# Performance work log

Hardware: AMD Instinct MI355X
Metric: run time of the kernel (lower is better)

## Reference

```python
import jax, jax.numpy as jnp
import numpy as np

D_K = 64  # d_model=512 // n_heads=8, hardcoded in source
NEG = -1e9


def setup_inputs() -> dict:
    key = jax.random.key(0)
    kq, kk, kv, km = jax.random.split(key, 4)
    B, H, S, D = 2, 8, 2048, D_K
    Q = jax.random.normal(kq, (B, H, S, D), dtype=jnp.float32)
    K = jax.random.normal(kk, (B, H, S, D), dtype=jnp.float32)
    V = jax.random.normal(kv, (B, H, S, D), dtype=jnp.float32)
    attn_mask = jax.random.randint(km, (B, H, S, S), 0, 2).astype(jnp.bool_)
    return {"Q": Q, "K": K, "V": V, "attn_mask": attn_mask}


def reference(Q, K, V, attn_mask):
    # scores = Q @ (K^T / sqrt(d_k))  -- scale applied to K^T as in source
    scale = 1.0 / np.sqrt(D_K).astype(np.float32)
    scores = jnp.einsum('bhqd,bhkd->bhqk', Q, K * scale)
    scores = jnp.where(attn_mask, NEG, scores)
    attn = jax.nn.softmax(scores, axis=-1)
    context = jnp.einsum('bhqk,bhkd->bhqd', attn, V)
    return (context, attn)
```

## Files before the change

kernel.cpp:

```cpp
#include <hip/hip_runtime.h>

typedef float f32x4 __attribute__((ext_vector_type(4)));
typedef _Float16 f16x4 __attribute__((ext_vector_type(4)));
typedef unsigned int u32x4 __attribute__((ext_vector_type(4)));
typedef __bf16 bf16x8_t __attribute__((ext_vector_type(8)));
typedef __bf16 bf16x4_t __attribute__((ext_vector_type(4)));

#define DEVFN static __device__ __forceinline__

constexpr int BHN = 16;
constexpr int SN  = 2048;
constexpr int DN  = 64;
constexpr size_t CTXN = (size_t)BHN * SN * DN;
constexpr int NK1 = 4;
constexpr int NK2 = 4;

DEVFN void qk4_mfma(f32x4& dA, f32x4& dB, bf16x8_t k0v, bf16x8_t k1v,
                    bf16x8_t qA0, bf16x8_t qA1, bf16x8_t qB0, bf16x8_t qB1) {
  asm volatile("s_nop 3\n\t"
               "v_mfma_f32_16x16x32_bf16 %0, %2, %4, %0\n\t"
               "v_mfma_f32_16x16x32_bf16 %1, %2, %6, %1\n\t"
               "v_mfma_f32_16x16x32_bf16 %0, %3, %5, %0\n\t"
               "v_mfma_f32_16x16x32_bf16 %1, %3, %7, %1\n\t"
               "s_nop 7\n\ts_nop 7"
               : "+v"(dA), "+v"(dB)
               : "v"(k0v), "v"(k1v), "v"(qA0), "v"(qA1), "v"(qB0), "v"(qB1));
}

DEVFN void pv8_mfma(f32x4& a0, f32x4& a1, f32x4& a2, f32x4& a3,
                    f32x4& b0, f32x4& b1, f32x4& b2, f32x4& b3,
                    bf16x4_t paA, bf16x4_t paB,
                    bf16x4_t v0, bf16x4_t v1, bf16x4_t v2, bf16x4_t v3) {
  asm volatile("s_nop 3\n\t"
               "v_mfma_f32_16x16x16_bf16 %0, %8, %10, %0\n\t"
               "v_mfma_f32_16x16x16_bf16 %4, %9, %10, %4\n\t"
               "v_mfma_f32_16x16x16_bf16 %1, %8, %11, %1\n\t"
               "v_mfma_f32_16x16x16_bf16 %5, %9, %11, %5\n\t"
               "v_mfma_f32_16x16x16_bf16 %2, %8, %12, %2\n\t"
               "v_mfma_f32_16x16x16_bf16 %6, %9, %12, %6\n\t"
               "v_mfma_f32_16x16x16_bf16 %3, %8, %13, %3\n\t"
               "v_mfma_f32_16x16x16_bf16 %7, %9, %13, %7\n\t"
               "s_nop 7\n\ts_nop 7"
               : "+v"(a0), "+v"(a1), "+v"(a2), "+v"(a3),
                 "+v"(b0), "+v"(b1), "+v"(b2), "+v"(b3)
               : "v"(paA), "v"(paB), "v"(v0), "v"(v1), "v"(v2), "v"(v3));
}

constexpr int PB = 2048, QB = 1024, KB = 1024, VB = 256;

__global__ __launch_bounds__(256) void prep_kernel(
    const void* __restrict__ mraw, unsigned int* __restrict__ bmT,
    const float* __restrict__ Q, const float* __restrict__ K,
    const float* __restrict__ V, __bf16* __restrict__ Qb,
    __bf16* __restrict__ Kb, __bf16* __restrict__ Vt) {
  const int bid = blockIdx.x;
  const int tidl = threadIdx.x;
  if (bid < PB) {
    __shared__ unsigned int sfl;
    if (tidl == 0) sfl = 0;
    __syncthreads();
    {
      unsigned int f = 0;
      const unsigned int* m32 = (const unsigned int*)mraw;
      for (int i = tidl; i < 4096; i += 256) {
        unsigned int w = m32[i];
        if (w == 0x3F800000u) f |= 2u;
        else if (w > 1u) f |= 1u;
      }
      if (f) atomicOr(&sfl, f);
    }
    __syncthreads();
    const unsigned int fl = (sfl & 2u) ? 2u : ((sfl & 1u) ? 1u : 0u);
    const int tid = bid * 256 + tidl;
    const int NT  = PB * 256;
    if (fl != 1u) {
      const int W = BHN * (SN / 32) * SN;
      const unsigned int* m32 = (const unsigned int*)mraw;
      for (int w = tid; w < W; w += NT) {
        const int q   = w & (SN - 1);
        const int kc2 = (w >> 11) & (SN / 32 - 1);
        const int bh  = w >> 17;
        const unsigned int* src = m32 + ((size_t)(bh * SN + q) * SN) + kc2 * 32;
        unsigned int r = 0;
        #pragma unroll
        for (int j = 0; j < 8; ++j) {
          u32x4 v = *(const u32x4*)(src + j * 4);
          r |= ((unsigned)(v[0] != 0u)) << (4 * j)
             | ((unsigned)(v[1] != 0u)) << (4 * j + 1)
             | ((unsigned)(v[2] != 0u)) << (4 * j + 2)
             | ((unsigned)(v[3] != 0u)) << (4 * j + 3);
        }
        bmT[w] = r;
      }
    } else {
      const int W4 = BHN * (SN / 128) * SN;
      const unsigned char* m8 = (const unsigned char*)mraw;
      for (int w4 = tid; w4 < W4; w4 += NT) {
        const int q   = w4 & (SN - 1);
        const int kc8 = (w4 >> 11) & (SN / 128 - 1);
        const int bh  = w4 >> 15;
        const unsigned char* src = m8 + ((size_t)(bh * SN + q) * SN) + kc8 * 128;
        #pragma unroll
        for (int i = 0; i < 4; ++i) {
          const unsigned int* s32 = (const unsigned int*)(src + 32 * i);
          unsigned int r = 0;
          #pragma unroll
          for (int j = 0; j < 8; ++j) {
            unsigned int x = s32[j];
            r |= ((unsigned)((x & 0x000000FFu) != 0u)) << (4 * j)
               | ((unsigned)((x & 0x0000FF00u) != 0u)) << (4 * j + 1)
               | ((unsigned)((x & 0x00FF0000u) != 0u)) << (4 * j + 2)
               | ((unsigned)((x & 0xFF000000u) != 0u)) << (4 * j + 3);
          }
          bmT[((size_t)(bh * (SN / 32) + kc8 * 4 + i)) * SN + q] = r;
        }
      }
    }
  } else if (bid < PB + QB + KB) {
    const bool isK = (bid >= PB + QB);
    const int rb = bid - (isK ? PB + QB : PB);
    const float* src = isK ? K : Q;
    __bf16* dst = isK ? Kb : Qb;
    const float scale = isK ? 0.125f : 1.0f;
    const size_t i = ((size_t)rb * 256 + tidl) * 8;
    f32x4 v0 = *(const f32x4*)(src + i);
    f32x4 v1 = *(const f32x4*)(src + i + 4);
    bf16x8_t o;
    o[0]=(__bf16)(v0[0]*scale); o[1]=(__bf16)(v0[1]*scale);
    o[2]=(__bf16)(v0[2]*scale); o[3]=(__bf16)(v0[3]*scale);
    o[4]=(__bf16)(v1[0]*scale); o[5]=(__bf16)(v1[1]*scale);
    o[6]=(__bf16)(v1[2]*scale); o[7]=(__bf16)(v1[3]*scale);
    *(bf16x8_t*)(dst + i) = o;
  } else {
    const int vb = bid - (PB + QB + KB);
    const int lane = tidl & 63, wv = tidl >> 6;
    const int k0 = ((vb & 15) * 4 + wv) * 32;
    const int bh = vb >> 4;
    const float* src = V + (size_t)bh * SN * DN;
    __bf16* dst = Vt + (((size_t)bh * (SN / 32) + (k0 >> 5)) * DN + lane) * 32;
    bf16x8_t w0, w1, w2, w3;
    #pragma unroll
    for (int i = 0; i < 8; ++i) {
      w0[i] = (__bf16)src[(size_t)(k0 + i) * DN + lane];
      w1[i] = (__bf16)src[(size_t)(k0 + 8 + i) * DN + lane];
      w2[i] = (__bf16)src[(size_t)(k0 + 16 + i) * DN + lane];
      w3[i] = (__bf16)src[(size_t)(k0 + 24 + i) * DN + lane];
    }
    *(bf16x8_t*)(dst)      = w0;
    *(bf16x8_t*)(dst + 8)  = w1;
    *(bf16x8_t*)(dst + 16) = w2;
    *(bf16x8_t*)(dst + 24) = w3;
  }
}

DEVFN void swz_decode(int bid, int& bh, int& c, int& x) {
  const int xcd = bid & 7, s8 = bid >> 3;
  bh = xcd + 8 * (s8 >> 6);
  const int r6 = s8 & 63;
  c = r6 >> 4;
  x = r6 & 15;
}

__global__ __launch_bounds__(256, 4) void attn_l_kernel(
    const __bf16* __restrict__ Qb, const __bf16* __restrict__ Kb,
    const unsigned int* __restrict__ bmT, float* __restrict__ lpart) {
  __shared__ __align__(16) char Ks[2][8192];
  const int tid = threadIdx.x;
  const int lane = tid & 63, wv = tid >> 6;
  const int qr = lane & 15, g = lane >> 4;
  int bh, c, x;
  swz_decode(blockIdx.x, bh, c, x);
  const int q0 = x * 128 + wv * 32;
  const int CS = SN / NK1, kbase = c * CS;
  const int NT = CS / 64;

  const __bf16* Qbb = Qb + (size_t)bh * SN * DN;
  const int qA = q0 + qr, qB = q0 + 16 + qr;
  bf16x8_t qfA0 = *(const bf16x8_t*)(Qbb + (size_t)qA * DN + 8 * g);
  bf16x8_t qfA1 = *(const bf16x8_t*)(Qbb + (size_t)qA * DN + 32 + 8 * g);
  bf16x8_t qfB0 = *(const bf16x8_t*)(Qbb + (size_t)qB * DN + 8 * g);
  bf16x8_t qfB1 = *(const bf16x8_t*)(Qbb + (size_t)qB * DN + 32 + 8 * g);
  const size_t rowA = (size_t)bh * SN + qA;
  const size_t rowB = (size_t)bh * SN + qB;
  const unsigned int* bmb = bmT + (size_t)bh * (SN / 32) * SN;
  const int kb2 = kbase >> 5;

  const int krow = tid >> 2;
  const int kcol = (tid & 3) * 32;
  const int swz  = (krow & 7) << 4;
  const int kdst0 = krow * 128 + ((kcol     ) ^ swz);
  const int kdst1 = krow * 128 + ((kcol + 16) ^ swz);
  const char* Ksrc = (const char*)(Kb + (size_t)bh * SN * DN + (size_t)kbase * DN);

  {
    u32x4 a = *(const u32x4*)(Ksrc + krow * 128 + kcol);
    u32x4 b = *(const u32x4*)(Ksrc + krow * 128 + kcol + 16);
    *(u32x4*)&Ks[0][kdst0] = a;
    *(u32x4*)&Ks[0][kdst1] = b;
  }
  __syncthreads();

  float lA = 0.f, lB = 0.f;
  for (int tt = 0; tt < NT; ++tt) {
    const bool pf = (tt + 1 < NT);
    u32x4 a, b;
    if (pf) {
      a = *(const u32x4*)(Ksrc + (tt + 1) * 8192 + krow * 128 + kcol);
      b = *(const u32x4*)(Ksrc + (tt + 1) * 8192 + krow * 128 + kcol + 16);
    }
    const char* Kbuf = Ks[tt & 1];
    const unsigned int wA0 = bmb[(size_t)(kb2 + 2 * tt    ) * SN + qA];
    const unsigned int wA1 = bmb[(size_t)(kb2 + 2 * tt + 1) * SN + qA];
    const unsigned int wB0 = bmb[(size_t)(kb2 + 2 * tt    ) * SN + qB];
    const unsigned int wB1 = bmb[(size_t)(kb2 + 2 * tt + 1) * SN + qB];
    #pragma unroll
    for (int s = 0; s < 4; ++s) {
      const int rk = 16 * s + qr;
      const int rsw = (rk & 7) << 4;
      bf16x8_t kf0 = *(const bf16x8_t*)&Kbuf[rk * 128 + ((16 * g     ) ^ rsw)];
      bf16x8_t kf1 = *(const bf16x8_t*)&Kbuf[rk * 128 + ((64 + 16 * g) ^ rsw)];
      f32x4 aA = {0,0,0,0}, aB = {0,0,0,0};
      qk4_mfma(aA, aB, kf0, kf1, qfA0, qfA1, qfB0, qfB1);
      const unsigned int wmA = (s < 2) ? wA0 : wA1;
      const unsigned int wmB = (s < 2) ? wB0 : wB1;
      const int sh = (s & 1) * 16 + 4 * g;
      lA += ((wmA >> (sh + 0)) & 1u) ? 0.f : __expf(aA[0]);
      lA += ((wmA >> (sh + 1)) & 1u) ? 0.f : __expf(aA[1]);
      lA += ((wmA >> (sh + 2)) & 1u) ? 0.f : __expf(aA[2]);
      lA += ((wmA >> (sh + 3)) & 1u) ? 0.f : __expf(aA[3]);
      lB += ((wmB >> (sh + 0)) & 1u) ? 0.f : __expf(aB[0]);
      lB += ((wmB >> (sh + 1)) & 1u) ? 0.f : __expf(aB[1]);
      lB += ((wmB >> (sh + 2)) & 1u) ? 0.f : __expf(aB[2]);
      lB += ((wmB >> (sh + 3)) & 1u) ? 0.f : __expf(aB[3]);
    }
    if (pf) {
      char* Kn = Ks[(tt + 1) & 1];
      *(u32x4*)&Kn[kdst0] = a;
      *(u32x4*)&Kn[kdst1] = b;
    }
    __syncthreads();
  }
  lA = lA + __shfl_xor(lA, 16); lA = lA + __shfl_xor(lA, 32);
  lB = lB + __shfl_xor(lB, 16); lB = lB + __shfl_xor(lB, 32);
  if (g == 0) {
    lpart[rowA * NK1 + c] = lA;
    lpart[rowB * NK1 + c] = lB;
  }
}

__global__ __launch_bounds__(256, 4) void attn_out_kernel(
    const __bf16* __restrict__ Qb, const __bf16* __restrict__ Kb,
    const __bf16* __restrict__ Vt, const unsigned int* __restrict__ bmT,
    const float* __restrict__ lpart, _Float16* __restrict__ cp,
    float* __restrict__ attn) {
  __shared__ __align__(16) char Ks[2][4096];
  __shared__ __align__(16) char Vs[2][4096];
  const int tid = threadIdx.x;
  const int lane = tid & 63, wv = tid >> 6;
  const int qr = lane & 15, g = lane >> 4;
  int bh, c, x;
  swz_decode(blockIdx.x, bh, c, x);
  const int q0 = x * 128 + wv * 32;
  const int CS = SN / NK2, kbase = c * CS;
  const int NT = CS / 32;

  const __bf16* Qbb = Qb + (size_t)bh * SN * DN;
  const int qA = q0 + qr, qB = q0 + 16 + qr;
  bf16x8_t qfA0 = *(const bf16x8_t*)(Qbb + (size_t)qA * DN + 8 * g);
  bf16x8_t qfA1 = *(const bf16x8_t*)(Qbb + (size_t)qA * DN + 32 + 8 * g);
  bf16x8_t qfB0 = *(const bf16x8_t*)(Qbb + (size_t)qB * DN + 8 * g);
  bf16x8_t qfB1 = *(const bf16x8_t*)(Qbb + (size_t)qB * DN + 32 + 8 * g);
  const size_t rowA = (size_t)bh * SN + qA;
  const size_t rowB = (size_t)bh * SN + qB;
  f32x4 l4A = *(const f32x4*)(lpart + rowA * NK1);
  f32x4 l4B = *(const f32x4*)(lpart + rowB * NK1);
  const float rlA = 1.0f / (l4A[0] + l4A[1] + l4A[2] + l4A[3]);
  const float rlB = 1.0f / (l4B[0] + l4B[1] + l4B[2] + l4B[3]);
  const unsigned int* bmb = bmT + (size_t)bh * (SN / 32) * SN;
  float* arowA = attn + rowA * SN;
  float* arowB = attn + rowB * SN;

  const int krow = tid >> 3;
  const int kcolb = (tid & 7) * 16;
  const int kdst = krow * 128 + (kcolb ^ ((krow & 7) << 4));
  const char* Ksrc = (const char*)(Kb + (size_t)bh * SN * DN + (size_t)kbase * DN);
  const int vd = tid >> 2;
  const int vkb = (tid & 3) * 16;
  const int vdst0 = vd * 64 + ((vkb    ) ^ ((vd & 7) << 3));
  const int vdst1 = vd * 64 + ((vkb + 8) ^ ((vd & 7) << 3));
  const char* Vsrc = (const char*)Vt + ((size_t)bh * (SN / 32) + (kbase >> 5)) * 4096;

  f32x4 cA0 = {0,0,0,0}, cA1 = {0,0,0,0}, cA2 = {0,0,0,0}, cA3 = {0,0,0,0};
  f32x4 cB0 = {0,0,0,0}, cB1 = {0,0,0,0}, cB2 = {0,0,0,0}, cB3 = {0,0,0,0};

  {
    u32x4 kr = *(const u32x4*)(Ksrc + krow * 128 + kcolb);
    u32x4 vr = *(const u32x4*)(Vsrc + tid * 16);
    *(u32x4*)&Ks[0][kdst] = kr;
    *(unsigned long long*)&Vs[0][vdst0] =
        ((unsigned long long)vr[1] << 32) | vr[0];
    *(unsigned long long*)&Vs[0][vdst1] =
        ((unsigned long long)vr[3] << 32) | vr[2];
  }
  __syncthreads();

  for (int tt = 0; tt < NT; ++tt) {
    const bool pf = (tt + 1 < NT);
    u32x4 kr, vr;
    if (pf) {
      kr = *(const u32x4*)(Ksrc + (tt + 1) * 4096 + krow * 128 + kcolb);
      vr = *(const u32x4*)(Vsrc + (tt + 1) * 4096 + tid * 16);
    }
    const char* Kbuf = Ks[tt & 1];
    const char* Vbuf = Vs[tt & 1];
    const int ktg = kbase + tt * 32;
    const unsigned int wmA = bmb[(size_t)((kbase >> 5) + tt) * SN + qA];
    const unsigned int wmB = bmb[(size_t)((kbase >> 5) + tt) * SN + qB];
    #pragma unroll
    for (int s = 0; s < 2; ++s) {
      const int rk = 16 * s + qr;
      bf16x8_t kf0 = *(const bf16x8_t*)&Kbuf[rk * 128 + ((16 * g     ) ^ ((rk & 7) << 4))];
      bf16x8_t kf1 = *(const bf16x8_t*)&Kbuf[rk * 128 + ((64 + 16 * g) ^ ((rk & 7) << 4))];
      const int vxor = (32 * s + 8 * g) ^ ((qr & 7) << 3);
      bf16x4_t vf0 = *(const bf16x4_t*)&Vbuf[(qr     ) * 64 + vxor];
      bf16x4_t vf1 = *(const bf16x4_t*)&Vbuf[(qr + 16) * 64 + vxor];
      bf16x4_t vf2 = *(const bf16x4_t*)&Vbuf[(qr + 32) * 64 + vxor];
      bf16x4_t vf3 = *(const bf16x4_t*)&Vbuf[(qr + 48) * 64 + vxor];
      f32x4 aA = {0,0,0,0}, aB = {0,0,0,0};
      qk4_mfma(aA, aB, kf0, kf1, qfA0, qfA1, qfB0, qfB1);
      const int sh = 16 * s + 4 * g;
      float pA0 = (((wmA >> (sh + 0)) & 1u) ? 0.f : __expf(aA[0])) * rlA;
      float pA1 = (((wmA >> (sh + 1)) & 1u) ? 0.f : __expf(aA[1])) * rlA;
      float pA2 = (((wmA >> (sh + 2)) & 1u) ? 0.f : __expf(aA[2])) * rlA;
      float pA3 = (((wmA >> (sh + 3)) & 1u) ? 0.f : __expf(aA[3])) * rlA;
      float pB0 = (((wmB >> (sh + 0)) & 1u) ? 0.f : __expf(aB[0])) * rlB;
      float pB1 = (((wmB >> (sh + 1)) & 1u) ? 0.f : __expf(aB[1])) * rlB;
      float pB2 = (((wmB >> (sh + 2)) & 1u) ? 0.f : __expf(aB[2])) * rlB;
      float pB3 = (((wmB >> (sh + 3)) & 1u) ? 0.f : __expf(aB[3])) * rlB;
      *(f32x4*)(arowA + ktg + sh) = (f32x4){pA0, pA1, pA2, pA3};
      *(f32x4*)(arowB + ktg + sh) = (f32x4){pB0, pB1, pB2, pB3};
      bf16x4_t paA = {(__bf16)pA0, (__bf16)pA1, (__bf16)pA2, (__bf16)pA3};
      bf16x4_t paB = {(__bf16)pB0, (__bf16)pB1, (__bf16)pB2, (__bf16)pB3};
      pv8_mfma(cA0, cA1, cA2, cA3, cB0, cB1, cB2, cB3, paA, paB, vf0, vf1, vf2, vf3);
    }
    if (pf) {
      char* Kn = Ks[(tt + 1) & 1];
      char* Vn = Vs[(tt + 1) & 1];
      *(u32x4*)&Kn[kdst] = kr;
      *(unsigned long long*)&Vn[vdst0] = ((unsigned long long)vr[1] << 32) | vr[0];
      *(unsigned long long*)&Vn[vdst1] = ((unsigned long long)vr[3] << 32) | vr[2];
    }
    __syncthreads();
  }
  _Float16* cdst = cp + (size_t)c * CTXN;
  const size_t baseo = (size_t)bh * SN * DN;
  #pragma unroll
  for (int j = 0; j < 4; ++j) {
    const size_t rA = baseo + (size_t)(q0 + 4 * g + j) * DN + qr;
    const size_t rB = baseo + (size_t)(q0 + 16 + 4 * g + j) * DN + qr;
    cdst[rA]      = (_Float16)cA0[j];
    cdst[rA + 16] = (_Float16)cA1[j];
    cdst[rA + 32] = (_Float16)cA2[j];
    cdst[rA + 48] = (_Float16)cA3[j];
    cdst[rB]      = (_Float16)cB0[j];
    cdst[rB + 16] = (_Float16)cB1[j];
    cdst[rB + 32] = (_Float16)cB2[j];
    cdst[rB + 48] = (_Float16)cB3[j];
  }
}

__global__ __launch_bounds__(256) void ctx_reduce_kernel(
    const _Float16* __restrict__ cp, float* __restrict__ ctx) {
  const size_t i = ((size_t)blockIdx.x * 256 + threadIdx.x) * 4;
  f16x4 a = *(const f16x4*)(cp + i);
  f16x4 b = *(const f16x4*)(cp + CTXN + i);
  f16x4 d = *(const f16x4*)(cp + 2 * CTXN + i);
  f16x4 e = *(const f16x4*)(cp + 3 * CTXN + i);
  f32x4 s;
  #pragma unroll
  for (int k = 0; k < 4; ++k)
    s[k] = ((float)a[k] + (float)b[k]) + ((float)d[k] + (float)e[k]);
  __builtin_nontemporal_store(s, (f32x4*)(ctx + i));
}

extern "C" void kernel_launch(void* const* d_in, const int* in_sizes, int n_in,
                              void* d_out, int out_size, void* d_ws, size_t ws_size,
                              hipStream_t stream) {
  const float* Q = (const float*)d_in[0];
  const float* K = (const float*)d_in[1];
  const float* V = (const float*)d_in[2];
  const void*  mraw = d_in[3];

  float* out  = (float*)d_out;
  float* ctx  = out;
  float* attn = out + CTXN;

  char* wsb = (char*)d_ws;
  unsigned int* bmT = (unsigned int*)(wsb + 256);
  float* lp   = (float*)(wsb + 256 + 8388608);
  __bf16* Qb  = (__bf16*)(wsb + 256 + 8388608 + 524288);
  __bf16* Kb  = (__bf16*)(wsb + 256 + 8388608 + 524288 + 4194304);
  __bf16* Vt  = (__bf16*)(wsb + 256 + 8388608 + 524288 + 2 * 4194304);
  _Float16* cp = (_Float16*)(wsb + 256 + 8388608 + 524288 + 3 * 4194304);

  prep_kernel<<<PB + QB + KB + VB, 256, 0, stream>>>(mraw, bmT, Q, K, V, Qb, Kb, Vt);
  attn_l_kernel<<<1024, 256, 0, stream>>>(Qb, Kb, bmT, lp);
  attn_out_kernel<<<1024, 256, 0, stream>>>(Qb, Kb, Vt, bmT, lp, cp, attn);
  ctx_reduce_kernel<<<2048, 256, 0, stream>>>(cp, ctx);
}
```

Before: 202.5 us.

## Fuse Q/K bf16 conversion into attention kernels; add nontemporal mask loads and attn stores

Drops the separate Q/K fp32-to-bf16 conversion blocks from the prep kernel. Both attention kernels now read fp32 Q and K directly and convert them (scaling K) on the fly when filling registers or shared memory. This saves a pass over Q and K plus the intermediate bf16 buffers, but doubles the global bytes each attention block loads for K and Q tiles and adds conversion ALU work in the loop. It also makes the mask reads in prep and the large attn-matrix writes nontemporal, to reduce cache pollution.

```diff
diff --git a/kernel.cpp b/kernel.cpp
--- a/kernel.cpp
+++ b/kernel.cpp
@@ -14,6 +14,7 @@
 constexpr size_t CTXN = (size_t)BHN * SN * DN;
 constexpr int NK1 = 4;
 constexpr int NK2 = 4;
+constexpr float SCL = 0.125f;
 
 DEVFN void qk4_mfma(f32x4& dA, f32x4& dB, bf16x8_t k0v, bf16x8_t k1v,
                     bf16x8_t qA0, bf16x8_t qA1, bf16x8_t qB0, bf16x8_t qB1) {
@@ -46,13 +47,21 @@
                : "v"(paA), "v"(paB), "v"(v0), "v"(v1), "v"(v2), "v"(v3));
 }
 
-constexpr int PB = 2048, QB = 1024, KB = 1024, VB = 256;
+DEVFN bf16x8_t cvt8(f32x4 a, f32x4 b, float s) {
+  bf16x8_t r;
+  r[0]=(__bf16)(a[0]*s); r[1]=(__bf16)(a[1]*s); r[2]=(__bf16)(a[2]*s); r[3]=(__bf16)(a[3]*s);
+  r[4]=(__bf16)(b[0]*s); r[5]=(__bf16)(b[1]*s); r[6]=(__bf16)(b[2]*s); r[7]=(__bf16)(b[3]*s);
+  return r;
+}
+DEVFN bf16x8_t ldq8(const float* p) {
+  return cvt8(*(const f32x4*)p, *(const f32x4*)(p + 4), 1.0f);
+}
+
+constexpr int PB = 2048, VB = 256;
 
 __global__ __launch_bounds__(256) void prep_kernel(
     const void* __restrict__ mraw, unsigned int* __restrict__ bmT,
-    const float* __restrict__ Q, const float* __restrict__ K,
-    const float* __restrict__ V, __bf16* __restrict__ Qb,
-    __bf16* __restrict__ Kb, __bf16* __restrict__ Vt) {
+    const float* __restrict__ V, __bf16* __restrict__ Vt) {
   const int bid = blockIdx.x;
   const int tidl = threadIdx.x;
   if (bid < PB) {
@@ -84,7 +93,7 @@
         unsigned int r = 0;
         #pragma unroll
         for (int j = 0; j < 8; ++j) {
-          u32x4 v = *(const u32x4*)(src + j * 4);
+          u32x4 v = __builtin_nontemporal_load((const u32x4*)(src + j * 4));
           r |= ((unsigned)(v[0] != 0u)) << (4 * j)
              | ((unsigned)(v[1] != 0u)) << (4 * j + 1)
              | ((unsigned)(v[2] != 0u)) << (4 * j + 2)
@@ -116,23 +125,8 @@
         }
       }
     }
-  } else if (bid < PB + QB + KB) {
-    const bool isK = (bid >= PB + QB);
-    const int rb = bid - (isK ? PB + QB : PB);
-    const float* src = isK ? K : Q;
-    __bf16* dst = isK ? Kb : Qb;
-    const float scale = isK ? 0.125f : 1.0f;
-    const size_t i = ((size_t)rb * 256 + tidl) * 8;
-    f32x4 v0 = *(const f32x4*)(src + i);
-    f32x4 v1 = *(const f32x4*)(src + i + 4);
-    bf16x8_t o;
-    o[0]=(__bf16)(v0[0]*scale); o[1]=(__bf16)(v0[1]*scale);
-    o[2]=(__bf16)(v0[2]*scale); o[3]=(__bf16)(v0[3]*scale);
-    o[4]=(__bf16)(v1[0]*scale); o[5]=(__bf16)(v1[1]*scale);
-    o[6]=(__bf16)(v1[2]*scale); o[7]=(__bf16)(v1[3]*scale);
-    *(bf16x8_t*)(dst + i) = o;
   } else {
-    const int vb = bid - (PB + QB + KB);
+    const int vb = bid - PB;
     const int lane = tidl & 63, wv = tidl >> 6;
     const int k0 = ((vb & 15) * 4 + wv) * 32;
     const int bh = vb >> 4;
@@ -162,7 +156,7 @@
 }
 
 __global__ __launch_bounds__(256, 4) void attn_l_kernel(
-    const __bf16* __restrict__ Qb, const __bf16* __restrict__ Kb,
+    const float* __restrict__ Q, const float* __restrict__ K,
     const unsigned int* __restrict__ bmT, float* __restrict__ lpart) {
   __shared__ __align__(16) char Ks[2][8192];
   const int tid = threadIdx.x;
@@ -174,39 +168,45 @@
   const int CS = SN / NK1, kbase = c * CS;
   const int NT = CS / 64;
 
-  const __bf16* Qbb = Qb + (size_t)bh * SN * DN;
+  const float* Qbb = Q + (size_t)bh * SN * DN;
   const int qA = q0 + qr, qB = q0 + 16 + qr;
-  bf16x8_t qfA0 = *(const bf16x8_t*)(Qbb + (size_t)qA * DN + 8 * g);
-  bf16x8_t qfA1 = *(const bf16x8_t*)(Qbb + (size_t)qA * DN + 32 + 8 * g);
-  bf16x8_t qfB0 = *(const bf16x8_t*)(Qbb + (size_t)qB * DN + 8 * g);
-  bf16x8_t qfB1 = *(const bf16x8_t*)(Qbb + (size_t)qB * DN + 32 + 8 * g);
+  bf16x8_t qfA0 = ldq8(Qbb + (size_t)qA * DN + 8 * g);
+  bf16x8_t qfA1 = ldq8(Qbb + (size_t)qA * DN + 32 + 8 * g);
+  bf16x8_t qfB0 = ldq8(Qbb + (size_t)qB * DN + 8 * g);
+  bf16x8_t qfB1 = ldq8(Qbb + (size_t)qB * DN + 32 + 8 * g);
   const size_t rowA = (size_t)bh * SN + qA;
   const size_t rowB = (size_t)bh * SN + qB;
   const unsigned int* bmb = bmT + (size_t)bh * (SN / 32) * SN;
   const int kb2 = kbase >> 5;
 
   const int krow = tid >> 2;
-  const int kcol = (tid & 3) * 32;
+  const int kc   = (tid & 3) * 16;
   const int swz  = (krow & 7) << 4;
-  const int kdst0 = krow * 128 + ((kcol     ) ^ swz);
-  const int kdst1 = krow * 128 + ((kcol + 16) ^ swz);
-  const char* Ksrc = (const char*)(Kb + (size_t)bh * SN * DN + (size_t)kbase * DN);
+  const int kdst0 = krow * 128 + (((tid & 3) * 32     ) ^ swz);
+  const int kdst1 = krow * 128 + (((tid & 3) * 32 + 16) ^ swz);
+  const float* Ksrc = K + (size_t)bh * SN * DN + (size_t)kbase * DN
+                        + krow * 64 + kc;
 
   {
-    u32x4 a = *(const u32x4*)(Ksrc + krow * 128 + kcol);
-    u32x4 b = *(const u32x4*)(Ksrc + krow * 128 + kcol + 16);
-    *(u32x4*)&Ks[0][kdst0] = a;
-    *(u32x4*)&Ks[0][kdst1] = b;
+    f32x4 a0 = *(const f32x4*)(Ksrc);
+    f32x4 a1 = *(const f32x4*)(Ksrc + 4);
+    f32x4 a2 = *(const f32x4*)(Ksrc + 8);
+    f32x4 a3 = *(const f32x4*)(Ksrc + 12);
+    *(bf16x8_t*)&Ks[0][kdst0] = cvt8(a0, a1, SCL);
+    *(bf16x8_t*)&Ks[0][kdst1] = cvt8(a2, a3, SCL);
   }
   __syncthreads();
 
   float lA = 0.f, lB = 0.f;
   for (int tt = 0; tt < NT; ++tt) {
     const bool pf = (tt + 1 < NT);
-    u32x4 a, b;
+    f32x4 a0, a1, a2, a3;
     if (pf) {
-      a = *(const u32x4*)(Ksrc + (tt + 1) * 8192 + krow * 128 + kcol);
-      b = *(const u32x4*)(Ksrc + (tt + 1) * 8192 + krow * 128 + kcol + 16);
+      const float* s = Ksrc + (tt + 1) * 4096;
+      a0 = *(const f32x4*)(s);
+      a1 = *(const f32x4*)(s + 4);
+      a2 = *(const f32x4*)(s + 8);
+      a3 = *(const f32x4*)(s + 12);
     }
     const char* Kbuf = Ks[tt & 1];
     const unsigned int wA0 = bmb[(size_t)(kb2 + 2 * tt    ) * SN + qA];
@@ -235,8 +235,8 @@
     }
     if (pf) {
       char* Kn = Ks[(tt + 1) & 1];
-      *(u32x4*)&Kn[kdst0] = a;
-      *(u32x4*)&Kn[kdst1] = b;
+      *(bf16x8_t*)&Kn[kdst0] = cvt8(a0, a1, SCL);
+      *(bf16x8_t*)&Kn[kdst1] = cvt8(a2, a3, SCL);
     }
     __syncthreads();
   }
@@ -249,7 +249,7 @@
 }
 
 __global__ __launch_bounds__(256, 4) void attn_out_kernel(
-    const __bf16* __restrict__ Qb, const __bf16* __restrict__ Kb,
+    const float* __restrict__ Q, const float* __restrict__ K,
     const __bf16* __restrict__ Vt, const unsigned int* __restrict__ bmT,
     const float* __restrict__ lpart, _Float16* __restrict__ cp,
     float* __restrict__ attn) {
@@ -264,12 +264,12 @@
   const int CS = SN / NK2, kbase = c * CS;
   const int NT = CS / 32;
 
-  const __bf16* Qbb = Qb + (size_t)bh * SN * DN;
+  const float* Qbb = Q + (size_t)bh * SN * DN;
   const int qA = q0 + qr, qB = q0 + 16 + qr;
-  bf16x8_t qfA0 = *(const bf16x8_t*)(Qbb + (size_t)qA * DN + 8 * g);
-  bf16x8_t qfA1 = *(const bf16x8_t*)(Qbb + (size_t)qA * DN + 32 + 8 * g);
-  bf16x8_t qfB0 = *(const bf16x8_t*)(Qbb + (size_t)qB * DN + 8 * g);
-  bf16x8_t qfB1 = *(const bf16x8_t*)(Qbb + (size_t)qB * DN + 32 + 8 * g);
+  bf16x8_t qfA0 = ldq8(Qbb + (size_t)qA * DN + 8 * g);
+  bf16x8_t qfA1 = ldq8(Qbb + (size_t)qA * DN + 32 + 8 * g);
+  bf16x8_t qfB0 = ldq8(Qbb + (size_t)qB * DN + 8 * g);
+  bf16x8_t qfB1 = ldq8(Qbb + (size_t)qB * DN + 32 + 8 * g);
   const size_t rowA = (size_t)bh * SN + qA;
   const size_t rowB = (size_t)bh * SN + qB;
   f32x4 l4A = *(const f32x4*)(lpart + rowA * NK1);
@@ -281,9 +281,10 @@
   float* arowB = attn + rowB * SN;
 
   const int krow = tid >> 3;
-  const int kcolb = (tid & 7) * 16;
-  const int kdst = krow * 128 + (kcolb ^ ((krow & 7) << 4));
-  const char* Ksrc = (const char*)(Kb + (size_t)bh * SN * DN + (size_t)kbase * DN);
+  const int kc   = (tid & 7) * 8;
+  const int kdst = krow * 128 + (((tid & 7) * 16) ^ ((krow & 7) << 4));
+  const float* Ksrc = K + (size_t)bh * SN * DN + (size_t)kbase * DN
+                        + krow * 64 + kc;
   const int vd = tid >> 2;
   const int vkb = (tid & 3) * 16;
   const int vdst0 = vd * 64 + ((vkb    ) ^ ((vd & 7) << 3));
@@ -294,9 +295,10 @@
   f32x4 cB0 = {0,0,0,0}, cB1 = {0,0,0,0}, cB2 = {0,0,0,0}, cB3 = {0,0,0,0};
 
   {
-    u32x4 kr = *(const u32x4*)(Ksrc + krow * 128 + kcolb);
+    f32x4 a0 = *(const f32x4*)(Ksrc);
+    f32x4 a1 = *(const f32x4*)(Ksrc + 4);
     u32x4 vr = *(const u32x4*)(Vsrc + tid * 16);
-    *(u32x4*)&Ks[0][kdst] = kr;
+    *(bf16x8_t*)&Ks[0][kdst] = cvt8(a0, a1, SCL);
     *(unsigned long long*)&Vs[0][vdst0] =
         ((unsigned long long)vr[1] << 32) | vr[0];
     *(unsigned long long*)&Vs[0][vdst1] =
@@ -306,9 +308,12 @@
 
   for (int tt = 0; tt < NT; ++tt) {
     const bool pf = (tt + 1 < NT);
-    u32x4 kr, vr;
+    f32x4 a0, a1;
+    u32x4 vr;
     if (pf) {
-      kr = *(const u32x4*)(Ksrc + (tt + 1) * 4096 + krow * 128 + kcolb);
+      const float* s = Ksrc + (tt + 1) * 2048;
+      a0 = *(const f32x4*)(s);
+      a1 = *(const f32x4*)(s + 4);
       vr = *(const u32x4*)(Vsrc + (tt + 1) * 4096 + tid * 16);
     }
     const char* Kbuf = Ks[tt & 1];
@@ -337,8 +342,10 @@
       float pB1 = (((wmB >> (sh + 1)) & 1u) ? 0.f : __expf(aB[1])) * rlB;
       float pB2 = (((wmB >> (sh + 2)) & 1u) ? 0.f : __expf(aB[2])) * rlB;
       float pB3 = (((wmB >> (sh + 3)) & 1u) ? 0.f : __expf(aB[3])) * rlB;
-      *(f32x4*)(arowA + ktg + sh) = (f32x4){pA0, pA1, pA2, pA3};
-      *(f32x4*)(arowB + ktg + sh) = (f32x4){pB0, pB1, pB2, pB3};
+      __builtin_nontemporal_store((f32x4){pA0, pA1, pA2, pA3},
+                                  (f32x4*)(arowA + ktg + sh));
+      __builtin_nontemporal_store((f32x4){pB0, pB1, pB2, pB3},
+                                  (f32x4*)(arowB + ktg + sh));
       bf16x4_t paA = {(__bf16)pA0, (__bf16)pA1, (__bf16)pA2, (__bf16)pA3};
       bf16x4_t paB = {(__bf16)pB0, (__bf16)pB1, (__bf16)pB2, (__bf16)pB3};
       pv8_mfma(cA0, cA1, cA2, cA3, cB0, cB1, cB2, cB3, paA, paB, vf0, vf1, vf2, vf3);
@@ -346,7 +353,7 @@
     if (pf) {
       char* Kn = Ks[(tt + 1) & 1];
       char* Vn = Vs[(tt + 1) & 1];
-      *(u32x4*)&Kn[kdst] = kr;
+      *(bf16x8_t*)&Kn[kdst] = cvt8(a0, a1, SCL);
       *(unsigned long long*)&Vn[vdst0] = ((unsigned long long)vr[1] << 32) | vr[0];
       *(unsigned long long*)&Vn[vdst1] = ((unsigned long long)vr[3] << 32) | vr[2];
     }
@@ -398,13 +405,11 @@
   char* wsb = (char*)d_ws;
   unsigned int* bmT = (unsigned int*)(wsb + 256);
   float* lp   = (float*)(wsb + 256 + 8388608);
-  __bf16* Qb  = (__bf16*)(wsb + 256 + 8388608 + 524288);
-  __bf16* Kb  = (__bf16*)(wsb + 256 + 8388608 + 524288 + 4194304);
-  __bf16* Vt  = (__bf16*)(wsb + 256 + 8388608 + 524288 + 2 * 4194304);
-  _Float16* cp = (_Float16*)(wsb + 256 + 8388608 + 524288 + 3 * 4194304);
-
-  prep_kernel<<<PB + QB + KB + VB, 256, 0, stream>>>(mraw, bmT, Q, K, V, Qb, Kb, Vt);
-  attn_l_kernel<<<1024, 256, 0, stream>>>(Qb, Kb, bmT, lp);
-  attn_out_kernel<<<1024, 256, 0, stream>>>(Qb, Kb, Vt, bmT, lp, cp, attn);
+  __bf16* Vt  = (__bf16*)(wsb + 256 + 8388608 + 524288);
+  _Float16* cp = (_Float16*)(wsb + 256 + 8388608 + 524288 + 4194304);
+
+  prep_kernel<<<PB + VB, 256, 0, stream>>>(mraw, bmT, V, Vt);
+  attn_l_kernel<<<1024, 256, 0, stream>>>(Q, K, bmT, lp);
+  attn_out_kernel<<<1024, 256, 0, stream>>>(Q, K, Vt, bmT, lp, cp, attn);
   ctx_reduce_kernel<<<2048, 256, 0, stream>>>(cp, ctx);
 }
```

After: 272.3 us. 34.5% more time.

## Use native exp2 with log2e-folded K scale and enlarge attention-pass key tiles

Applied to the files above, without the earlier changes.

Folds log2(e) into the K prescale so both kernels can compute softmax exponentials with raw v_exp_f32 (exp2) through inline asm. In the second pass the normalisation becomes a -log2(l) bias preloaded into the MFMA accumulator, which removes the per-element multiply by the reciprocal. The second kernel also moves from 32-key to 64-key tiles with larger double-buffered LDS and a new V swizzle, halving loop iterations and barriers. The cost is more LDS per block, which may lower occupancy, and extra exp2 rounding error from the folded scale.

```diff
diff --git a/kernel.cpp b/kernel.cpp
--- a/kernel.cpp
+++ b/kernel.cpp
@@ -12,8 +12,8 @@
 constexpr int SN  = 2048;
 constexpr int DN  = 64;
 constexpr size_t CTXN = (size_t)BHN * SN * DN;
-constexpr int NK1 = 4;
-constexpr int NK2 = 4;
+constexpr int NK = 4;
+constexpr float KSCL = 0.18033688f;
 
 DEVFN void qk4_mfma(f32x4& dA, f32x4& dB, bf16x8_t k0v, bf16x8_t k1v,
                     bf16x8_t qA0, bf16x8_t qA1, bf16x8_t qB0, bf16x8_t qB1) {
@@ -44,6 +44,15 @@
                : "+v"(a0), "+v"(a1), "+v"(a2), "+v"(a3),
                  "+v"(b0), "+v"(b1), "+v"(b2), "+v"(b3)
                : "v"(paA), "v"(paB), "v"(v0), "v"(v1), "v"(v2), "v"(v3));
+}
+
+DEVFN void exp2x4(float& a, float& b, float& c, float& d) {
+  asm volatile("v_exp_f32 %0, %0\n\t"
+               "v_exp_f32 %1, %1\n\t"
+               "v_exp_f32 %2, %2\n\t"
+               "v_exp_f32 %3, %3\n\t"
+               "s_nop 1"
+               : "+v"(a), "+v"(b), "+v"(c), "+v"(d));
 }
 
 constexpr int PB = 2048, QB = 1024, KB = 1024, VB = 256;
@@ -121,7 +130,7 @@
     const int rb = bid - (isK ? PB + QB : PB);
     const float* src = isK ? K : Q;
     __bf16* dst = isK ? Kb : Qb;
-    const float scale = isK ? 0.125f : 1.0f;
+    const float scale = isK ? KSCL : 1.0f;
     const size_t i = ((size_t)rb * 256 + tidl) * 8;
     f32x4 v0 = *(const f32x4*)(src + i);
     f32x4 v1 = *(const f32x4*)(src + i + 4);
@@ -171,7 +180,7 @@
   int bh, c, x;
   swz_decode(blockIdx.x, bh, c, x);
   const int q0 = x * 128 + wv * 32;
-  const int CS = SN / NK1, kbase = c * CS;
+  const int CS = SN / NK, kbase = c * CS;
   const int NT = CS / 64;
 
   const __bf16* Qbb = Qb + (size_t)bh * SN * DN;
@@ -224,14 +233,18 @@
       const unsigned int wmA = (s < 2) ? wA0 : wA1;
       const unsigned int wmB = (s < 2) ? wB0 : wB1;
       const int sh = (s & 1) * 16 + 4 * g;
-      lA += ((wmA >> (sh + 0)) & 1u) ? 0.f : __expf(aA[0]);
-      lA += ((wmA >> (sh + 1)) & 1u) ? 0.f : __expf(aA[1]);
-      lA += ((wmA >> (sh + 2)) & 1u) ? 0.f : __expf(aA[2]);
-      lA += ((wmA >> (sh + 3)) & 1u) ? 0.f : __expf(aA[3]);
-      lB += ((wmB >> (sh + 0)) & 1u) ? 0.f : __expf(aB[0]);
-      lB += ((wmB >> (sh + 1)) & 1u) ? 0.f : __expf(aB[1]);
-      lB += ((wmB >> (sh + 2)) & 1u) ? 0.f : __expf(aB[2]);
-      lB += ((wmB >> (sh + 3)) & 1u) ? 0.f : __expf(aB[3]);
+      float eA0 = aA[0], eA1 = aA[1], eA2 = aA[2], eA3 = aA[3];
+      float eB0 = aB[0], eB1 = aB[1], eB2 = aB[2], eB3 = aB[3];
+      exp2x4(eA0, eA1, eA2, eA3);
+      exp2x4(eB0, eB1, eB2, eB3);
+      lA += ((wmA >> (sh + 0)) & 1u) ? 0.f : eA0;
+      lA += ((wmA >> (sh + 1)) & 1u) ? 0.f : eA1;
+      lA += ((wmA >> (sh + 2)) & 1u) ? 0.f : eA2;
+      lA += ((wmA >> (sh + 3)) & 1u) ? 0.f : eA3;
+      lB += ((wmB >> (sh + 0)) & 1u) ? 0.f : eB0;
+      lB += ((wmB >> (sh + 1)) & 1u) ? 0.f : eB1;
+      lB += ((wmB >> (sh + 2)) & 1u) ? 0.f : eB2;
+      lB += ((wmB >> (sh + 3)) & 1u) ? 0.f : eB3;
     }
     if (pf) {
       char* Kn = Ks[(tt + 1) & 1];
@@ -243,8 +256,8 @@
   lA = lA + __shfl_xor(lA, 16); lA = lA + __shfl_xor(lA, 32);
   lB = lB + __shfl_xor(lB, 16); lB = lB + __shfl_xor(lB, 32);
   if (g == 0) {
-    lpart[rowA * NK1 + c] = lA;
-    lpart[rowB * NK1 + c] = lB;
+    lpart[rowA * NK + c] = lA;
+    lpart[rowB * NK + c] = lB;
   }
 }
 
@@ -253,16 +266,16 @@
     const __bf16* __restrict__ Vt, const unsigned int* __restrict__ bmT,
     const float* __restrict__ lpart, _Float16* __restrict__ cp,
     float* __restrict__ attn) {
-  __shared__ __align__(16) char Ks[2][4096];
-  __shared__ __align__(16) char Vs[2][4096];
+  __shared__ __align__(16) char Ks[2][8192];
+  __shared__ __align__(16) char Vs[2][8192];
   const int tid = threadIdx.x;
   const int lane = tid & 63, wv = tid >> 6;
   const int qr = lane & 15, g = lane >> 4;
   int bh, c, x;
   swz_decode(blockIdx.x, bh, c, x);
   const int q0 = x * 128 + wv * 32;
-  const int CS = SN / NK2, kbase = c * CS;
-  const int NT = CS / 32;
+  const int CS = SN / NK, kbase = c * CS;
+  const int NT = CS / 64;
 
   const __bf16* Qbb = Qb + (size_t)bh * SN * DN;
   const int qA = q0 + qr, qB = q0 + 16 + qr;
@@ -272,73 +285,91 @@
   bf16x8_t qfB1 = *(const bf16x8_t*)(Qbb + (size_t)qB * DN + 32 + 8 * g);
   const size_t rowA = (size_t)bh * SN + qA;
   const size_t rowB = (size_t)bh * SN + qB;
-  f32x4 l4A = *(const f32x4*)(lpart + rowA * NK1);
-  f32x4 l4B = *(const f32x4*)(lpart + rowB * NK1);
-  const float rlA = 1.0f / (l4A[0] + l4A[1] + l4A[2] + l4A[3]);
-  const float rlB = 1.0f / (l4B[0] + l4B[1] + l4B[2] + l4B[3]);
+  f32x4 l4A = *(const f32x4*)(lpart + rowA * NK);
+  f32x4 l4B = *(const f32x4*)(lpart + rowB * NK);
+  const float lg2A = -__log2f(l4A[0] + l4A[1] + l4A[2] + l4A[3]);
+  const float lg2B = -__log2f(l4B[0] + l4B[1] + l4B[2] + l4B[3]);
   const unsigned int* bmb = bmT + (size_t)bh * (SN / 32) * SN;
   float* arowA = attn + rowA * SN;
   float* arowB = attn + rowB * SN;
-
-  const int krow = tid >> 3;
-  const int kcolb = (tid & 7) * 16;
-  const int kdst = krow * 128 + (kcolb ^ ((krow & 7) << 4));
+  const int kb2 = kbase >> 5;
+
+  const int krow = tid >> 2;
+  const int kcol = (tid & 3) * 32;
+  const int kswz = (krow & 7) << 4;
+  const int kdst0 = krow * 128 + ((kcol     ) ^ kswz);
+  const int kdst1 = krow * 128 + ((kcol + 16) ^ kswz);
   const char* Ksrc = (const char*)(Kb + (size_t)bh * SN * DN + (size_t)kbase * DN);
   const int vd = tid >> 2;
   const int vkb = (tid & 3) * 16;
-  const int vdst0 = vd * 64 + ((vkb    ) ^ ((vd & 7) << 3));
-  const int vdst1 = vd * 64 + ((vkb + 8) ^ ((vd & 7) << 3));
+  const int vswz = (vd & 15) << 3;
+  const int vbase = vd * 128;
   const char* Vsrc = (const char*)Vt + ((size_t)bh * (SN / 32) + (kbase >> 5)) * 4096;
 
   f32x4 cA0 = {0,0,0,0}, cA1 = {0,0,0,0}, cA2 = {0,0,0,0}, cA3 = {0,0,0,0};
   f32x4 cB0 = {0,0,0,0}, cB1 = {0,0,0,0}, cB2 = {0,0,0,0}, cB3 = {0,0,0,0};
 
   {
-    u32x4 kr = *(const u32x4*)(Ksrc + krow * 128 + kcolb);
-    u32x4 vr = *(const u32x4*)(Vsrc + tid * 16);
-    *(u32x4*)&Ks[0][kdst] = kr;
-    *(unsigned long long*)&Vs[0][vdst0] =
-        ((unsigned long long)vr[1] << 32) | vr[0];
-    *(unsigned long long*)&Vs[0][vdst1] =
-        ((unsigned long long)vr[3] << 32) | vr[2];
+    u32x4 ka = *(const u32x4*)(Ksrc + krow * 128 + kcol);
+    u32x4 kb = *(const u32x4*)(Ksrc + krow * 128 + kcol + 16);
+    u32x4 va = *(const u32x4*)(Vsrc + vd * 64 + vkb);
+    u32x4 vb = *(const u32x4*)(Vsrc + 4096 + vd * 64 + vkb);
+    *(u32x4*)&Ks[0][kdst0] = ka;
+    *(u32x4*)&Ks[0][kdst1] = kb;
+    *(unsigned long long*)&Vs[0][vbase + ((vkb     ) ^ vswz)] = ((unsigned long long)va[1] << 32) | va[0];
+    *(unsigned long long*)&Vs[0][vbase + ((vkb +  8) ^ vswz)] = ((unsigned long long)va[3] << 32) | va[2];
+    *(unsigned long long*)&Vs[0][vbase + ((64 + vkb    ) ^ vswz)] = ((unsigned long long)vb[1] << 32) | vb[0];
+    *(unsigned long long*)&Vs[0][vbase + ((64 + vkb + 8) ^ vswz)] = ((unsigned long long)vb[3] << 32) | vb[2];
   }
   __syncthreads();
 
   for (int tt = 0; tt < NT; ++tt) {
     const bool pf = (tt + 1 < NT);
-    u32x4 kr, vr;
+    u32x4 ka, kb, va, vb;
     if (pf) {
-      kr = *(const u32x4*)(Ksrc + (tt + 1) * 4096 + krow * 128 + kcolb);
-      vr = *(const u32x4*)(Vsrc + (tt + 1) * 4096 + tid * 16);
+      ka = *(const u32x4*)(Ksrc + (tt + 1) * 8192 + krow * 128 + kcol);
+      kb = *(const u32x4*)(Ksrc + (tt + 1) * 8192 + krow * 128 + kcol + 16);
+      va = *(const u32x4*)(Vsrc + (tt + 1) * 8192 + vd * 64 + vkb);
+      vb = *(const u32x4*)(Vsrc + (tt + 1) * 8192 + 4096 + vd * 64 + vkb);
     }
     const char* Kbuf = Ks[tt & 1];
     const char* Vbuf = Vs[tt & 1];
-    const int ktg = kbase + tt * 32;
-    const unsigned int wmA = bmb[(size_t)((kbase >> 5) + tt) * SN + qA];
-    const unsigned int wmB = bmb[(size_t)((kbase >> 5) + tt) * SN + qB];
+    const int ktg = kbase + tt * 64;
+    const unsigned int wA0 = bmb[(size_t)(kb2 + 2 * tt    ) * SN + qA];
+    const unsigned int wA1 = bmb[(size_t)(kb2 + 2 * tt + 1) * SN + qA];
+    const unsigned int wB0 = bmb[(size_t)(kb2 + 2 * tt    ) * SN + qB];
+    const unsigned int wB1 = bmb[(size_t)(kb2 + 2 * tt + 1) * SN + qB];
     #pragma unroll
-    for (int s = 0; s < 2; ++s) {
+    for (int s = 0; s < 4; ++s) {
       const int rk = 16 * s + qr;
-      bf16x8_t kf0 = *(const bf16x8_t*)&Kbuf[rk * 128 + ((16 * g     ) ^ ((rk & 7) << 4))];
-      bf16x8_t kf1 = *(const bf16x8_t*)&Kbuf[rk * 128 + ((64 + 16 * g) ^ ((rk & 7) << 4))];
-      const int vxor = (32 * s + 8 * g) ^ ((qr & 7) << 3);
-      bf16x4_t vf0 = *(const bf16x4_t*)&Vbuf[(qr     ) * 64 + vxor];
-      bf16x4_t vf1 = *(const bf16x4_t*)&Vbuf[(qr + 16) * 64 + vxor];
-      bf16x4_t vf2 = *(const bf16x4_t*)&Vbuf[(qr + 32) * 64 + vxor];
-      bf16x4_t vf3 = *(const bf16x4_t*)&Vbuf[(qr + 48) * 64 + vxor];
-      f32x4 aA = {0,0,0,0}, aB = {0,0,0,0};
+      const int rsw = (rk & 7) << 4;
+      bf16x8_t kf0 = *(const bf16x8_t*)&Kbuf[rk * 128 + ((16 * g     ) ^ rsw)];
+      bf16x8_t kf1 = *(const bf16x8_t*)&Kbuf[rk * 128 + ((64 + 16 * g) ^ rsw)];
+      const int vxor = (32 * s + 8 * g) ^ (qr << 3);
+      bf16x4_t vf0 = *(const bf16x4_t*)&Vbuf[(qr     ) * 128 + vxor];
+      bf16x4_t vf1 = *(const bf16x4_t*)&Vbuf[(qr + 16) * 128 + vxor];
+      bf16x4_t vf2 = *(const bf16x4_t*)&Vbuf[(qr + 32) * 128 + vxor];
+      bf16x4_t vf3 = *(const bf16x4_t*)&Vbuf[(qr + 48) * 128 + vxor];
+      f32x4 aA = {lg2A, lg2A, lg2A, lg2A};
+      f32x4 aB = {lg2B, lg2B, lg2B, lg2B};
       qk4_mfma(aA, aB, kf0, kf1, qfA0, qfA1, qfB0, qfB1);
-      const int sh = 16 * s + 4 * g;
-      float pA0 = (((wmA >> (sh + 0)) & 1u) ? 0.f : __expf(aA[0])) * rlA;
-      float pA1 = (((wmA >> (sh + 1)) & 1u) ? 0.f : __expf(aA[1])) * rlA;
-      float pA2 = (((wmA >> (sh + 2)) & 1u) ? 0.f : __expf(aA[2])) * rlA;
-      float pA3 = (((wmA >> (sh + 3)) & 1u) ? 0.f : __expf(aA[3])) * rlA;
-      float pB0 = (((wmB >> (sh + 0)) & 1u) ? 0.f : __expf(aB[0])) * rlB;
-      float pB1 = (((wmB >> (sh + 1)) & 1u) ? 0.f : __expf(aB[1])) * rlB;
-      float pB2 = (((wmB >> (sh + 2)) & 1u) ? 0.f : __expf(aB[2])) * rlB;
-      float pB3 = (((wmB >> (sh + 3)) & 1u) ? 0.f : __expf(aB[3])) * rlB;
-      *(f32x4*)(arowA + ktg + sh) = (f32x4){pA0, pA1, pA2, pA3};
-      *(f32x4*)(arowB + ktg + sh) = (f32x4){pB0, pB1, pB2, pB3};
+      const unsigned int wmA = (s < 2) ? wA0 : wA1;
+      const unsigned int wmB = (s < 2) ? wB0 : wB1;
+      const int sh = (s & 1) * 16 + 4 * g;
+      float pA0 = aA[0], pA1 = aA[1], pA2 = aA[2], pA3 = aA[3];
+      float pB0 = aB[0], pB1 = aB[1], pB2 = aB[2], pB3 = aB[3];
+      exp2x4(pA0, pA1, pA2, pA3);
+      exp2x4(pB0, pB1, pB2, pB3);
+      pA0 = ((wmA >> (sh + 0)) & 1u) ? 0.f : pA0;
+      pA1 = ((wmA >> (sh + 1)) & 1u) ? 0.f : pA1;
+      pA2 = ((wmA >> (sh + 2)) & 1u) ? 0.f : pA2;
+      pA3 = ((wmA >> (sh + 3)) & 1u) ? 0.f : pA3;
+      pB0 = ((wmB >> (sh + 0)) & 1u) ? 0.f : pB0;
+      pB1 = ((wmB >> (sh + 1)) & 1u) ? 0.f : pB1;
+      pB2 = ((wmB >> (sh + 2)) & 1u) ? 0.f : pB2;
+      pB3 = ((wmB >> (sh + 3)) & 1u) ? 0.f : pB3;
+      *(f32x4*)(arowA + ktg + 16 * s + 4 * g) = (f32x4){pA0, pA1, pA2, pA3};
+      *(f32x4*)(arowB + ktg + 16 * s + 4 * g) = (f32x4){pB0, pB1, pB2, pB3};
       bf16x4_t paA = {(__bf16)pA0, (__bf16)pA1, (__bf16)pA2, (__bf16)pA3};
       bf16x4_t paB = {(__bf16)pB0, (__bf16)pB1, (__bf16)pB2, (__bf16)pB3};
       pv8_mfma(cA0, cA1, cA2, cA3, cB0, cB1, cB2, cB3, paA, paB, vf0, vf1, vf2, vf3);
@@ -346,9 +377,12 @@
     if (pf) {
       char* Kn = Ks[(tt + 1) & 1];
       char* Vn = Vs[(tt + 1) & 1];
-      *(u32x4*)&Kn[kdst] = kr;
-      *(unsigned long long*)&Vn[vdst0] = ((unsigned long long)vr[1] << 32) | vr[0];
-      *(unsigned long long*)&Vn[vdst1] = ((unsigned long long)vr[3] << 32) | vr[2];
+      *(u32x4*)&Kn[kdst0] = ka;
+      *(u32x4*)&Kn[kdst1] = kb;
+      *(unsigned long long*)&Vn[vbase + ((vkb     ) ^ vswz)] = ((unsigned long long)va[1] << 32) | va[0];
+      *(unsigned long long*)&Vn[vbase + ((vkb +  8) ^ vswz)] = ((unsigned long long)va[3] << 32) | va[2];
+      *(unsigned long long*)&Vn[vbase + ((64 + vkb    ) ^ vswz)] = ((unsigned long long)vb[1] << 32) | vb[0];
+      *(unsigned long long*)&Vn[vbase + ((64 + vkb + 8) ^ vswz)] = ((unsigned long long)vb[3] << 32) | vb[2];
     }
     __syncthreads();
   }
```

Measured after the change: 250.8 us. 23.8% more time.
